# Kernel optimization log

Hardware: AMD Instinct MI355X
Metric: run time of the kernel (lower is better)

The kernel has to match this reference:

```python
import jax, jax.numpy as jnp
import numpy as np
from jax import lax

K = 8
SCALE = 100.0

# ---- straight-through binarizers (match torch custom Functions) ----
@jax.custom_vjp
def bin_w(x):
    return jnp.sign(x)

def _bin_w_fwd(x):
    return jnp.sign(x), None

def _bin_w_bwd(_, g):
    return (g,)  # identity STE

bin_w.defvjp(_bin_w_fwd, _bin_w_bwd)

@jax.custom_vjp
def bin_a(x):
    return jnp.sign(x)

def _bin_a_fwd(x):
    return jnp.sign(x), x

def _bin_a_bwd(x, g):
    return (g * jnp.clip(2.0 - jnp.abs(2.0 * x), 0.0, None),)

bin_a.defvjp(_bin_a_fwd, _bin_a_bwd)

# ---- SDP sampling with custom backward (grad_z scaled by sqrt(scale)) ----
@jax.custom_vjp
def sdp(m, z, rv):
    # m: (N,), z: (K,N), rv: (1,K) -> w: (N,)
    return (rv @ z)[0] + m

def _sdp_fwd(m, z, rv):
    return (rv @ z)[0] + m, rv

def _sdp_bwd(rv, g):
    grad_m = g
    grad_z = (rv.T @ g[None, :]) * np.sqrt(SCALE)  # (K,N)
    return (grad_m, grad_z, jnp.zeros_like(rv))

sdp.defvjp(_sdp_fwd, _sdp_bwd)

def _forward(x, M, Z, alpha, rv):
    N = M.size
    m = M.reshape(N)          # (N,)
    z = Z.reshape(K, N)       # (K,N)
    # no_grad normalization of m,z data: value changes, gradient passes through identity
    A = m * m + jnp.sum(z * z, axis=0) / SCALE
    inv = lax.rsqrt(A)
    m_used = m + lax.stop_gradient(m * inv - m)
    z_used = z + lax.stop_gradient(z * inv - z)
    w = sdp(m_used, z_used, rv)               # (N,)
    bw = bin_w(w).reshape(M.shape)            # (O,I,3,3) in {-1,+1}
    ba = bin_a(x)                             # (B,C,H,W) in {-1,+1}
    out = lax.conv_general_dilated(
        ba, bw, window_strides=(1, 1), padding=((1, 1), (1, 1)),
        dimension_numbers=('NCHW', 'OIHW', 'NCHW'))
    return out * alpha  # alpha (O,1,1) broadcasts over (B,O,H,W)

def setup_inputs() -> dict:
    key = jax.random.key(0)
    k1, k2, k3, k4, k5 = jax.random.split(key, 5)
    x = jax.random.normal(k1, (64, 256, 28, 28), dtype=jnp.float32)
    M = jax.random.normal(k2, (256, 256, 3, 3), dtype=jnp.float32)
    Z = jax.random.normal(k3, (8, 256, 256, 3, 3), dtype=jnp.float32)
    alpha = jax.random.uniform(k4, (256, 1, 1), dtype=jnp.float32)
    rv = jax.random.normal(k5, (1, 8), dtype=jnp.float32) * np.float32(1.0 / np.sqrt(SCALE))
    return {"x": x, "M": M, "Z": Z, "alpha": alpha, "rv": rv}

def reference(x, M, Z, alpha, rv):
    return _forward(x, M, Z, alpha, rv)
```

## Files before the change

### kernel.cpp

```cpp
#include <hip/hip_runtime.h>
#include <stdint.h>

typedef unsigned int uint32;

#define BB 64
#define CC 256
#define OO 256
#define HH 28
#define WW 28
#define HWP 784
#define NWT 589824

__global__ __launch_bounds__(256) void pack_x_kernel(
    const float* __restrict__ x, uint32* __restrict__ apack) {
  int p = blockIdx.x * 256 + threadIdx.x;
  int j = blockIdx.y;
  int b = blockIdx.z;
  if (p >= HWP) return;
  const float* xp = x + ((size_t)(b * CC + j * 32) * HWP) + p;
  uint32 m = 0;
#pragma unroll
  for (int cc = 0; cc < 32; ++cc) {
    float v = xp[(size_t)cc * HWP];
    m |= ((uint32)(v > 0.0f)) << cc;
  }
  apack[((size_t)b * HWP + p) * 8 + j] = m;
}

__global__ __launch_bounds__(256) void pack_w_kernel(
    const float* __restrict__ M, const float* __restrict__ Z,
    const float* __restrict__ rv, uint32* __restrict__ wpack) {
  __shared__ float sacc[576];
  const int o = blockIdx.x;
  const int jh = blockIdx.y;
  const int tid = threadIdx.x;
  const size_t base = (size_t)o * 2304 + (size_t)jh * 576;

  float r[8];
#pragma unroll
  for (int k = 0; k < 8; ++k) r[k] = rv[k];

#pragma unroll
  for (int ii = 0; ii < 3; ++ii) {
    int i = tid + ii * 256;
    if (i < 576) {
      float s = M[base + i];
#pragma unroll
      for (int k = 0; k < 8; ++k) s += r[k] * Z[(size_t)k * NWT + base + i];
      sacc[i] = s;
    }
  }
  __syncthreads();

  if (tid < 18) {
    int tap = tid % 9;
    int jj = tid / 9;
    uint32 m = 0;
#pragma unroll
    for (int cc = 0; cc < 32; ++cc) {
      float v = sacc[(jj * 32 + cc) * 9 + tap];
      m |= ((uint32)(v > 0.0f)) << cc;
    }
    wpack[(o * 9 + tap) * 8 + jh * 2 + jj] = m;
  }
}

__global__ __launch_bounds__(256) void ptab_kernel(
    const uint32* __restrict__ wpack, const float* __restrict__ alpha,
    float* __restrict__ ptabA, uint32* __restrict__ ptabP) {
  int o = threadIdx.x;
  const uint32* wt = wpack + (size_t)o * 72;
  int pt[9];
#pragma unroll
  for (int t = 0; t < 9; ++t) {
    int s = 0;
#pragma unroll
    for (int j = 0; j < 8; ++j) s += __popc(wt[t * 8 + j]);
    pt[t] = s;
  }
  int row0 = pt[0] + pt[1] + pt[2], row2 = pt[6] + pt[7] + pt[8];
  int col0 = pt[0] + pt[3] + pt[6], col2 = pt[2] + pt[5] + pt[8];
  float a = alpha[o];
  const int nv[9] = {4, 6, 4, 6, 9, 6, 4, 6, 4};
  int S[9];
  S[0] = row0 + col0 - pt[0]; S[1] = row0; S[2] = row0 + col2 - pt[2];
  S[3] = col0;                S[4] = 0;    S[5] = col2;
  S[6] = row2 + col0 - pt[6]; S[7] = row2; S[8] = row2 + col2 - pt[8];
#pragma unroll
  for (int c = 0; c < 9; ++c)
    ptabA[o * 9 + c] = a * (float)(256 * nv[c] + 2 * S[c]);
  ptabP[o * 4 + 0] = __float_as_uint(-2.0f * a);
  ptabP[o * 4 + 1] = (uint32)col0;
  ptabP[o * 4 + 2] = (uint32)col2;
  ptabP[o * 4 + 3] = 0;
}

#define BCNT_ACC(T, x) asm("v_bcnt_u32_b32 %0, %1, %0" : "+v"(T) : "v"(x))

__global__ __launch_bounds__(256, 8) void conv_kernel(
    const uint32* __restrict__ apack, const uint32* __restrict__ wpack,
    const float* __restrict__ ptabA, const uint32* __restrict__ ptabP,
    float* __restrict__ out) {
  __shared__ float atab[16 * 9];

  const int rg = blockIdx.x;
  const int og = blockIdx.y;
  const int b  = blockIdx.z;
  const int tid = threadIdx.x;
  const int lane = tid & 63;
  const int wv = tid >> 6;
  const int w = lane & 31;
  const int rb = rg * 16 + wv * 4 + (lane >> 5) * 2;
  const bool wact = w < WW;

  if (tid < 144) atab[tid] = ptabA[og * 144 + tid];
  __syncthreads();

  const int wcl = wact ? w : (WW - 1);
  uint4 A[4][2];
#pragma unroll
  for (int i = 0; i < 4; ++i) {
    int rr = rb - 1 + i;
    bool v = (rr >= 0) && (rr < HH);
    const uint4* src =
        (const uint4*)(apack + ((size_t)(b * HWP + (v ? rr : 0) * WW + wcl)) * 8);
    uint4 lo = src[0], hi = src[1];
    if (!v) { lo = make_uint4(0, 0, 0, 0); hi = make_uint4(0, 0, 0, 0); }
    A[i][0] = lo;
    A[i][1] = hi;
  }

  const int wc = (w == 0) ? 0 : (w == WW - 1 ? 2 : 1);
  const int r1v = rb + 1;
  const int hc0 = (rb == 0) ? 0 : (rb == HH - 1 ? 2 : 1);
  const int hc1 = (r1v == 0) ? 0 : (r1v == HH - 1 ? 2 : 1);
  const int cls0 = hc0 * 3 + wc;
  const int cls1 = hc1 * 3 + wc;

  const size_t obase = ((size_t)b * OO + og * 16) * HWP + (size_t)rb * WW + w;
  const bool st0 = wact && (rb < HH);
  const bool st1 = wact && (r1v < HH);

  for (int oi = 0; oi < 16; ++oi) {
    const int o = og * 16 + oi;
    const int wo = __builtin_amdgcn_readfirstlane(o * 72);
    const uint32* wt = wpack + wo;
    const uint4 pm = ((const uint4*)ptabP)[o];
    const float m = __uint_as_float(pm.x);

    uint32 T00 = 0, T01 = 0, T02 = 0, T10 = 0, T11 = 0, T12 = 0;
#pragma unroll
    for (int dh = 0; dh < 3; ++dh) {
      const uint32* a0 = (const uint32*)&A[dh][0];
      const uint32* a1 = (const uint32*)&A[dh + 1][0];
#pragma unroll
      for (int j = 0; j < 8; ++j) {
        const uint32 w0 = wt[(dh * 3 + 0) * 8 + j];
        const uint32 w1 = wt[(dh * 3 + 1) * 8 + j];
        const uint32 w2 = wt[(dh * 3 + 2) * 8 + j];
        const uint32 av0 = a0[j], av1 = a1[j];
        BCNT_ACC(T00, av0 ^ w0);
        BCNT_ACC(T01, av0 ^ w1);
        BCNT_ACC(T02, av0 ^ w2);
        BCNT_ACC(T10, av1 ^ w0);
        BCNT_ACC(T11, av1 ^ w1);
        BCNT_ACC(T12, av1 ^ w2);
      }
    }
    uint32 pl = __shfl_up(T00 | (T10 << 16), 1);
    uint32 pr = __shfl_down(T02 | (T12 << 16), 1);
    if (w == 0)      pl = pm.y * 0x10001u;
    if (w == WW - 1) pr = pm.z * 0x10001u;
    uint32 tp = pl + (T01 | (T11 << 16)) + pr;
    float r0 = fmaf(m, (float)(tp & 0xffffu), atab[oi * 9 + cls0]);
    float r1 = fmaf(m, (float)(tp >> 16), atab[oi * 9 + cls1]);
    if (st0) out[obase + (size_t)oi * HWP] = r0;
    if (st1) out[obase + (size_t)oi * HWP + WW] = r1;
  }
}

extern "C" void kernel_launch(void* const* d_in, const int* in_sizes, int n_in,
                              void* d_out, int out_size, void* d_ws,
                              size_t ws_size, hipStream_t stream) {
  const float* x     = (const float*)d_in[0];
  const float* M     = (const float*)d_in[1];
  const float* Z     = (const float*)d_in[2];
  const float* alpha = (const float*)d_in[3];
  const float* rv    = (const float*)d_in[4];
  float* out = (float*)d_out;

  uint32* apack = (uint32*)d_ws;
  uint32* wpack = (uint32*)((char*)d_ws + 1605632);
  float*  ptabA = (float*)((char*)d_ws + 1679360);
  uint32* ptabP = (uint32*)((char*)d_ws + 1688576);

  pack_x_kernel<<<dim3(4, 8, BB), 256, 0, stream>>>(x, apack);
  pack_w_kernel<<<dim3(256, 4), 256, 0, stream>>>(M, Z, rv, wpack);
  ptab_kernel<<<dim3(1), 256, 0, stream>>>(wpack, alpha, ptabA, ptabP);
  conv_kernel<<<dim3(2, 16, BB), 256, 0, stream>>>(apack, wpack, ptabA, ptabP,
                                                   out);
}
```

Before: 191.2 us.

## Replace XNOR-popcount conv with int8 MFMA implicit GEMM using ±1 bytes

Adds a new path that packs activations and weights as signed int8 (±1) in channel-last layouts and computes the convolution as an implicit GEMM with 16x16x64 int8 MFMA instructions. Input tiles are staged in shared memory with zero padding, and alpha is applied on output. This replaces the VALU bit-popcount kernel and the correction-table kernel. The path only runs if the workspace holds about 13 MB, otherwise it falls back to the old kernels. It uses 8x more activation bytes and reads weights from global memory without LDS staging.

```diff
diff --git a/kernel.cpp b/kernel.cpp
--- a/kernel.cpp
+++ b/kernel.cpp
@@ -2,6 +2,7 @@
 #include <stdint.h>
 
 typedef unsigned int uint32;
+typedef int v4i __attribute__((ext_vector_type(4)));
 
 #define BB 64
 #define CC 256
@@ -10,6 +11,160 @@
 #define WW 28
 #define HWP 784
 #define NWT 589824
+
+
+__global__ __launch_bounds__(256) void pack_a8_kernel(
+    const float* __restrict__ x, char* __restrict__ a8) {
+  __shared__ uint32 tt[56 * 65];
+  const int pg = blockIdx.x;
+  const int b = blockIdx.y;
+  const int tid = threadIdx.x;
+  const int p0 = pg * 56;
+  if (tid < 224) {
+    int px = tid % 56, g = tid / 56;
+    const float* xb = x + (size_t)b * CC * HWP + p0 + px;
+#pragma unroll
+    for (int ii = 0; ii < 16; ++ii) {
+      int c4 = g * 16 + ii;
+      uint32 wd = 0;
+#pragma unroll
+      for (int i = 0; i < 4; ++i) {
+        float v = xb[(size_t)(c4 * 4 + i) * HWP];
+        wd |= ((v > 0.0f) ? 0x01u : 0xFFu) << (8 * i);
+      }
+      tt[px * 65 + c4] = wd;
+    }
+  }
+  __syncthreads();
+  for (int j = tid; j < 56 * 64; j += 256) {
+    int px = j >> 6, c4 = j & 63;
+    ((uint32*)a8)[(((size_t)b * HWP + p0 + px) << 6) + c4] = tt[px * 65 + c4];
+  }
+}
+
+__global__ __launch_bounds__(256) void pack_w8_kernel(
+    const float* __restrict__ M, const float* __restrict__ Z,
+    const float* __restrict__ rv, char* __restrict__ w8t) {
+  __shared__ float sacc[576];
+  const int o = blockIdx.x;
+  const int jh = blockIdx.y;
+  const int tid = threadIdx.x;
+  const size_t base = (size_t)o * 2304 + (size_t)jh * 576;
+
+  float r[8];
+#pragma unroll
+  for (int k = 0; k < 8; ++k) r[k] = rv[k];
+
+#pragma unroll
+  for (int ii = 0; ii < 3; ++ii) {
+    int i = tid + ii * 256;
+    if (i < 576) {
+      float s = M[base + i];
+#pragma unroll
+      for (int k = 0; k < 8; ++k) s += r[k] * Z[(size_t)k * NWT + base + i];
+      sacc[i] = s;
+    }
+  }
+  __syncthreads();
+
+  for (int t = tid; t < 576; t += 256) {
+    int tap = t % 9, cl = t / 9;
+    w8t[(size_t)o * 2304 + tap * 256 + jh * 64 + cl] =
+        (sacc[cl * 9 + tap] > 0.0f) ? (char)1 : (char)-1;
+  }
+}
+
+#define CBYTES 272
+#define TROWS 6
+#define PPMAX (TROWS * 30)
+
+__global__ __launch_bounds__(256, 4) void conv_mfma(
+    const char* __restrict__ a8, const char* __restrict__ w8t,
+    const float* __restrict__ alpha, float* __restrict__ out) {
+  __shared__ char At[PPMAX * CBYTES];
+  const int pxg = blockIdx.x;
+  const int b = blockIdx.y;
+  const int tid = threadIdx.x;
+  const int p0 = pxg * 64;
+  const int h0 = p0 / WW;
+
+  for (int i = tid; i < (PPMAX * CBYTES) / 16; i += 256)
+    ((uint4*)At)[i] = make_uint4(0, 0, 0, 0);
+  __syncthreads();
+
+  for (int lr = 0; lr < TROWS; ++lr) {
+    int r = h0 - 1 + lr;
+    if (r < 0 || r >= HH) continue;
+    for (int idx = tid; idx < 448; idx += 256) {
+      int w = idx >> 4, i16 = idx & 15;
+      uint4 v = *(const uint4*)(a8 +
+                 (((size_t)(b * HWP + r * WW + w)) << 8) + i16 * 16);
+      *(uint4*)(At + (lr * 30 + w + 1) * CBYTES + i16 * 16) = v;
+    }
+  }
+  __syncthreads();
+
+  const int lane = tid & 63, q = lane >> 4, n15 = lane & 15;
+  const int ob = (tid >> 6) * 64;
+
+  int av[4];
+  int wva[4];
+#pragma unroll
+  for (int nt = 0; nt < 4; ++nt) {
+    int p = p0 + nt * 16 + n15;
+    if (p > HWP - 1) p = HWP - 1;
+    int h = p / WW, w = p - h * WW;
+    av[nt] = ((h - h0 + 1) * 30 + w + 1 - 31) * CBYTES + q * 16;
+  }
+#pragma unroll
+  for (int mi = 0; mi < 4; ++mi)
+    wva[mi] = (ob + mi * 16 + n15) * 2304 + q * 16;
+
+  v4i acc[4][4];
+#pragma unroll
+  for (int i = 0; i < 4; ++i)
+#pragma unroll
+    for (int j = 0; j < 4; ++j) acc[i][j] = (v4i){0, 0, 0, 0};
+
+#pragma unroll 1
+  for (int tap = 0; tap < 9; ++tap) {
+    const int dh = tap / 3, dw = tap - dh * 3;
+    const int boff = (dh * 30 + dw) * CBYTES;
+    const int woff = tap * 256;
+#pragma unroll
+    for (int kc = 0; kc < 4; ++kc) {
+      v4i a[4], bf[4];
+#pragma unroll
+      for (int mi = 0; mi < 4; ++mi)
+        a[mi] = *(const v4i*)(w8t + wva[mi] + woff + kc * 64);
+#pragma unroll
+      for (int nt = 0; nt < 4; ++nt)
+        bf[nt] = *(const v4i*)(At + av[nt] + boff + kc * 64);
+#pragma unroll
+      for (int mi = 0; mi < 4; ++mi)
+#pragma unroll
+        for (int nt = 0; nt < 4; ++nt)
+          acc[mi][nt] = __builtin_amdgcn_mfma_i32_16x16x64_i8(
+              a[mi], bf[nt], acc[mi][nt], 0, 0, 0);
+    }
+  }
+
+#pragma unroll
+  for (int mi = 0; mi < 4; ++mi) {
+#pragma unroll
+    for (int reg = 0; reg < 4; ++reg) {
+      int o = ob + mi * 16 + q * 4 + reg;
+      float al = alpha[o];
+      size_t obase = ((size_t)b * OO + o) * HWP;
+#pragma unroll
+      for (int nt = 0; nt < 4; ++nt) {
+        int p = p0 + nt * 16 + n15;
+        if (p < HWP) out[obase + p] = al * (float)acc[mi][nt][reg];
+      }
+    }
+  }
+}
+
 
 __global__ __launch_bounds__(256) void pack_x_kernel(
     const float* __restrict__ x, uint32* __restrict__ apack) {
@@ -35,11 +190,9 @@
   const int jh = blockIdx.y;
   const int tid = threadIdx.x;
   const size_t base = (size_t)o * 2304 + (size_t)jh * 576;
-
   float r[8];
 #pragma unroll
   for (int k = 0; k < 8; ++k) r[k] = rv[k];
-
 #pragma unroll
   for (int ii = 0; ii < 3; ++ii) {
     int i = tid + ii * 256;
@@ -51,7 +204,6 @@
     }
   }
   __syncthreads();
-
   if (tid < 18) {
     int tap = tid % 9;
     int jj = tid / 9;
@@ -102,7 +254,6 @@
     const float* __restrict__ ptabA, const uint32* __restrict__ ptabP,
     float* __restrict__ out) {
   __shared__ float atab[16 * 9];
-
   const int rg = blockIdx.x;
   const int og = blockIdx.y;
   const int b  = blockIdx.z;
@@ -189,14 +340,21 @@
   const float* rv    = (const float*)d_in[4];
   float* out = (float*)d_out;
 
-  uint32* apack = (uint32*)d_ws;
-  uint32* wpack = (uint32*)((char*)d_ws + 1605632);
-  float*  ptabA = (float*)((char*)d_ws + 1679360);
-  uint32* ptabP = (uint32*)((char*)d_ws + 1688576);
-
-  pack_x_kernel<<<dim3(4, 8, BB), 256, 0, stream>>>(x, apack);
-  pack_w_kernel<<<dim3(256, 4), 256, 0, stream>>>(M, Z, rv, wpack);
-  ptab_kernel<<<dim3(1), 256, 0, stream>>>(wpack, alpha, ptabA, ptabP);
-  conv_kernel<<<dim3(2, 16, BB), 256, 0, stream>>>(apack, wpack, ptabA, ptabP,
-                                                   out);
-}
+  if (ws_size >= 13434880) {
+    char* a8  = (char*)d_ws;
+    char* w8t = (char*)d_ws + 12845056;
+    pack_a8_kernel<<<dim3(14, BB), 256, 0, stream>>>(x, a8);
+    pack_w8_kernel<<<dim3(256, 4), 256, 0, stream>>>(M, Z, rv, w8t);
+    conv_mfma<<<dim3(13, BB), 256, 0, stream>>>(a8, w8t, alpha, out);
+  } else {
+    uint32* apack = (uint32*)d_ws;
+    uint32* wpack = (uint32*)((char*)d_ws + 1605632);
+    float*  ptabA = (float*)((char*)d_ws + 1679360);
+    uint32* ptabP = (uint32*)((char*)d_ws + 1688576);
+    pack_x_kernel<<<dim3(4, 8, BB), 256, 0, stream>>>(x, apack);
+    pack_w_kernel<<<dim3(256, 4), 256, 0, stream>>>(M, Z, rv, wpack);
+    ptab_kernel<<<dim3(1), 256, 0, stream>>>(wpack, alpha, ptabA, ptabP);
+    conv_kernel<<<dim3(2, 16, BB), 256, 0, stream>>>(apack, wpack, ptabA,
+                                                     ptabP, out);
+  }
+}
```

Result: slower. 208.3 us (+8.9%).
